# Kernel optimization log

Measured on AMD Instinct MI355X. Metric: run time of the kernel, lower is better.

Reference implementation:

```python
import jax, jax.numpy as jnp
import numpy as np

# ---- config (matches init_kwargs) ----
NUM_HEADS = 8
HEAD_DIM = 48
IN_CH = 384
OUT_CH = 384
AGENTS_HW = (7, 7)
CLUSTERS_HW = (2, 2)
NUM_MODULES = 2          # ['PartitionalClustering', 'FuzzyClustering']
N_GROUPS = 1 + 2 * NUM_MODULES   # p + (k, v) per module
D = NUM_HEADS * HEAD_DIM          # 384
NUM_CLUSTERS = CLUSTERS_HW[0] * CLUSTERS_HW[1]   # 4 per module
NUM_ALL_CLUSTERS = NUM_MODULES * NUM_CLUSTERS    # 8
EPS = 1e-6


def adaptive_avg_pool(x, oh, ow):
    # x: [b, c, H, W], H % oh == 0, W % ow == 0 -> exact block mean
    b, c, H, W = x.shape
    return x.reshape(b, c, oh, H // oh, ow, W // ow).mean(axis=(3, 5))


def setup_inputs() -> dict:
    key = jax.random.key(0)
    ks = jax.random.split(key, 6)
    B, H, W = 16, 56, 56
    x = jax.random.normal(ks[0], (B, IN_CH, H, W), dtype=jnp.float32)
    # proj: 1x1 linear in_channels -> N_GROUPS * D
    proj_w = jax.random.normal(ks[1], (N_GROUPS * D, IN_CH), dtype=jnp.float32) * (IN_CH ** -0.5)
    proj_b = jnp.zeros((N_GROUPS * D,), dtype=jnp.float32)
    sim_alpha = jnp.ones((NUM_ALL_CLUSTERS,), dtype=jnp.float32)
    sim_beta = jnp.zeros((NUM_ALL_CLUSTERS,), dtype=jnp.float32)
    proj2_w = jax.random.normal(ks[2], (OUT_CH, D), dtype=jnp.float32) * (D ** -0.5)
    proj2_b = jnp.zeros((OUT_CH,), dtype=jnp.float32)
    return {"x": x, "proj_w": proj_w, "proj_b": proj_b,
            "sim_alpha": sim_alpha, "sim_beta": sim_beta,
            "proj2_w": proj2_w, "proj2_b": proj2_b}


def _cluster_attention(i, k, v, kc, vc):
    # k: [b, c, Na] agent keys; v: [b, Na, c] agent values
    # kc, vc: [b, M, c] cluster centroids (keys / values)
    c = k.shape[1]
    scores = jnp.einsum('bmc,bcn->bmn', kc, k) / jnp.sqrt(jnp.float32(c))  # [b, M, Na]
    if i == 0:  # PartitionalClustering: attend over tokens per centroid
        attn = jax.nn.softmax(scores, axis=-1)
        agg = jnp.einsum('bmn,bnc->bmc', attn, v)
    else:       # FuzzyClustering: soft membership over clusters, normalized average
        memb = jax.nn.softmax(scores, axis=1)                              # over clusters
        agg = jnp.einsum('bmn,bnc->bmc', memb, v) / (memb.sum(axis=-1, keepdims=True) + EPS)
    return agg + vc  # with_cluster_bias=True


def reference(x, proj_w, proj_b, sim_alpha, sim_beta, proj2_w, proj2_b):
    B, C, H, W = x.shape
    # proj (1x1 linear over channels)
    y = jnp.einsum('bchw,oc->bohw', x, proj_w) + proj_b[None, :, None, None]
    y = y.reshape(B, N_GROUPS, D, H, W).transpose(1, 0, 2, 3, 4)
    b = B * NUM_HEADS
    c = HEAD_DIM
    y = y.reshape(N_GROUPS, b, c, H, W)
    p, r = y[0], y[1:]
    r = r.reshape(NUM_MODULES, 2, b, c, H, W)

    ah, aw = AGENTS_HW
    na = ah * aw
    agg_list = []
    for i in range(NUM_MODULES):  # fixed small structural loop
        k_full, v_full = r[i, 0], r[i, 1]
        kc = adaptive_avg_pool(k_full, *CLUSTERS_HW).reshape(b, c, NUM_CLUSTERS).transpose(0, 2, 1)
        vc = adaptive_avg_pool(v_full, *CLUSTERS_HW).reshape(b, c, NUM_CLUSTERS).transpose(0, 2, 1)
        k = adaptive_avg_pool(k_full, ah, aw).reshape(b, c, na)             # [b, c, Na]
        v = adaptive_avg_pool(v_full, ah, aw).reshape(b, c, na).transpose(0, 2, 1)  # [b, Na, c]
        agg_list.append(_cluster_attention(i, k, v, kc, vc))
    agg = jnp.concatenate(agg_list, axis=1)  # [b, M_all, c]

    p_agents = adaptive_avg_pool(p, ah, aw).reshape(b, c, na)  # [b, c, Na]
    # cosine similarity between centroid aggregates and query tokens
    agg_n = agg / (jnp.linalg.norm(agg, axis=-1, keepdims=True) + EPS)
    p_n = p_agents / (jnp.linalg.norm(p_agents, axis=1, keepdims=True) + EPS)
    sim = jnp.einsum('bmc,bcn->bmn', agg_n, p_n)  # [b, M_all, Na]
    similarity = sim_alpha[None, :, None] * sim + sim_beta[None, :, None]
    assignment = jax.nn.softmax(similarity, axis=1)  # over clusters

    out = jnp.einsum('bmc,bmn->bcn', agg, assignment)  # [b, c, Na]
    out = out.reshape(b, c, ah, aw)
    # bilinear upsample (half-pixel centers == torch align_corners=False)
    out = jax.image.resize(out, (b, c, H, W), method='linear')
    out = out.reshape(B, D, H, W)
    out = jnp.einsum('bdhw,od->bohw', out, proj2_w) + proj2_b[None, :, None, None]
    return out
```

## Files before the change

kernel.cpp:

```cpp
#include <hip/hip_runtime.h>
#include <math.h>

#define CIN    384
#define NPIX   3136

typedef float vf4 __attribute__((ext_vector_type(4)));
typedef __attribute__((ext_vector_type(4))) float f32x4;
typedef __attribute__((ext_vector_type(8))) short bf16x8;
typedef __attribute__((ext_vector_type(8))) unsigned short u16x8;

__device__ __forceinline__ unsigned short f2bf(float f) {
    unsigned u = __float_as_uint(f);
    u = (u + 0x7FFF + ((u >> 16) & 1)) >> 16;
    return (unsigned short)u;
}
__device__ __forceinline__ float bf2f(unsigned short h) {
    return __uint_as_float(((unsigned)h) << 16);
}

__global__ __launch_bounds__(256) void k_front(const float* __restrict__ x,
                                               const float* __restrict__ W1,
                                               const float* __restrict__ W2,
                                               unsigned short* __restrict__ Xhi,
                                               unsigned short* __restrict__ Xlo,
                                               unsigned short* __restrict__ Whi1,
                                               unsigned short* __restrict__ Wlo1,
                                               unsigned short* __restrict__ Whi2,
                                               unsigned short* __restrict__ Wlo2) {
    int blk = blockIdx.x;
    int t = threadIdx.x;
    if (blk >= 9024) {
        int i = (blk - 9024) * 256 + t;
        float w = W2[i];
        unsigned short hi = f2bf(w);
        Whi2[i] = hi;
        Wlo2[i] = f2bf(w - bf2f(hi));
        return;
    }
    if (blk >= 6144) {
        int i = (blk - 6144) * 256 + t;
        float w = W1[i];
        unsigned short hi = f2bf(w);
        Whi1[i] = hi;
        Wlo1[i] = f2bf(w - bf2f(hi));
        return;
    }
    int Bi = blk / CIN;
    int ch = blk - Bi * CIN;
    __shared__ float ps[56][14];
    __shared__ float s14[14][14];
    const float* xp = x + (size_t)(Bi * CIN + ch) * NPIX;
    for (int p = t; p < 784; p += 256) {
        int row = p / 14, cb = p % 14;
        const vf4 v = __builtin_nontemporal_load(
            reinterpret_cast<const vf4*>(xp + row * 56 + cb * 4));
        ps[row][cb] = v.x + v.y + v.z + v.w;
    }
    __syncthreads();
    if (t < 196) {
        int ri = t / 14, cb = t % 14;
        s14[ri][cb] = ps[4*ri][cb] + ps[4*ri+1][cb] + ps[4*ri+2][cb] + ps[4*ri+3][cb];
    }
    __syncthreads();
    if (t < 49) {
        int i = t / 7, j = t % 7;
        float s = (s14[2*i][2*j] + s14[2*i][2*j+1] + s14[2*i+1][2*j] + s14[2*i+1][2*j+1])
                  * (1.0f / 64.0f);
        int p = Bi * 49 + t;
        unsigned short hi = f2bf(s);
        Xhi[(size_t)p * 384 + ch] = hi;
        Xlo[(size_t)p * 384 + ch] = f2bf(s - bf2f(hi));
    } else if (t >= 64 && t < 68) {
        int m = t - 64;
        int mi = m / 2, mj = m % 2;
        float s = 0.f;
        for (int ri = 7*mi; ri < 7*mi + 7; ++ri)
            for (int cb = 7*mj; cb < 7*mj + 7; ++cb)
                s += s14[ri][cb];
        s *= (1.0f / 784.0f);
        int p = 784 + Bi * 4 + m;
        unsigned short hi = f2bf(s);
        Xhi[(size_t)p * 384 + ch] = hi;
        Xlo[(size_t)p * 384 + ch] = f2bf(s - bf2f(hi));
    }
}

__global__ __launch_bounds__(512) void k_fuse(
        const unsigned short* __restrict__ Whi, const unsigned short* __restrict__ Wlo,
        const unsigned short* __restrict__ Xhi, const unsigned short* __restrict__ Xlo,
        const float* __restrict__ proj_b,
        const float* __restrict__ alpha, const float* __restrict__ beta,
        unsigned short* __restrict__ osThi, unsigned short* __restrict__ osTlo) {
    int bb = blockIdx.x;
    int Bi = bb >> 3, head = bb & 7;
    __shared__ float yT[16560];
    __shared__ float e0[4][49], memb[4][49];
    __shared__ float msum[4];
    __shared__ float agg[8][48];
    __shared__ float anorm[8], pnorm[49];
    __shared__ float simL[8][49];
    __shared__ float assignW[8][49];
    unsigned short* sAh = (unsigned short*)yT;
    unsigned short* sAl = sAh + 9600;
    unsigned short* sBh = sAl + 9600;
    unsigned short* sBl = sBh + 2560;
    int t = threadIdx.x;
    int lane = t & 63, w = t >> 6;
    int fr = lane & 15, fq = lane >> 4;

    int row0 = t >> 2, ko0 = (t & 3) * 8;
    int g0 = row0 / 48, cc0 = row0 - g0 * 48;
    size_t aoff0 = (size_t)(g0 * 384 + head * 48 + cc0) * 384 + ko0;
    int c1 = t + 512;
    int row1 = c1 >> 2, ko1 = (c1 & 3) * 8;
    int g1 = row1 / 48, cc1 = row1 - g1 * 48;
    size_t aoff1 = (size_t)(g1 * 384 + head * 48 + cc1) * 384 + ko1;
    int bko = (t & 3) * 8;
    int brow = t >> 2;
    int bp = brow < 49 ? Bi * 49 + brow : 784 + Bi * 4 + (brow - 49);
    size_t boff = (size_t)bp * 384 + bko;

    u16x8 rAh0, rAl0, rAh1, rAl1, rBh, rBl;
    rAh0 = *(const u16x8*)(Whi + aoff0);
    rAl0 = *(const u16x8*)(Wlo + aoff0);
    if (t < 448) { rAh1 = *(const u16x8*)(Whi + aoff1); rAl1 = *(const u16x8*)(Wlo + aoff1); }
    if (t < 212) { rBh  = *(const u16x8*)(Xhi + boff);  rBl  = *(const u16x8*)(Xlo + boff); }

    f32x4 acc[2][4] = {};
    for (int step = 0; step < 12; ++step) {
        *(u16x8*)&sAh[row0 * 40 + ko0] = rAh0;
        *(u16x8*)&sAl[row0 * 40 + ko0] = rAl0;
        if (t < 448) {
            *(u16x8*)&sAh[row1 * 40 + ko1] = rAh1;
            *(u16x8*)&sAl[row1 * 40 + ko1] = rAl1;
        }
        if (t < 212) {
            *(u16x8*)&sBh[brow * 40 + bko] = rBh;
            *(u16x8*)&sBl[brow * 40 + bko] = rBl;
        }
        __syncthreads();
        if (step < 11) {
            int k0 = (step + 1) * 32;
            rAh0 = *(const u16x8*)(Whi + aoff0 + k0);
            rAl0 = *(const u16x8*)(Wlo + aoff0 + k0);
            if (t < 448) { rAh1 = *(const u16x8*)(Whi + aoff1 + k0); rAl1 = *(const u16x8*)(Wlo + aoff1 + k0); }
            if (t < 212) { rBh  = *(const u16x8*)(Xhi + boff + k0);  rBl  = *(const u16x8*)(Xlo + boff + k0); }
        }
        bf16x8 bh[4], bl[4];
#pragma unroll
        for (int nt = 0; nt < 4; ++nt) {
            int r = nt * 16 + fr;
            bh[nt] = *(const bf16x8*)&sBh[r * 40 + fq * 8];
            bl[nt] = *(const bf16x8*)&sBl[r * 40 + fq * 8];
        }
#pragma unroll
        for (int mi = 0; mi < 2; ++mi) {
            int mt = 2 * w + mi;
            if (mt < 15) {
                int r = mt * 16 + fr;
                bf16x8 ah = *(const bf16x8*)&sAh[r * 40 + fq * 8];
                bf16x8 al = *(const bf16x8*)&sAl[r * 40 + fq * 8];
#pragma unroll
                for (int nt = 0; nt < 4; ++nt) {
                    acc[mi][nt] = __builtin_amdgcn_mfma_f32_16x16x32_bf16(ah, bh[nt], acc[mi][nt], 0, 0, 0);
                    acc[mi][nt] = __builtin_amdgcn_mfma_f32_16x16x32_bf16(ah, bl[nt], acc[mi][nt], 0, 0, 0);
                    acc[mi][nt] = __builtin_amdgcn_mfma_f32_16x16x32_bf16(al, bh[nt], acc[mi][nt], 0, 0, 0);
                }
            }
        }
        __syncthreads();
    }
#pragma unroll
    for (int mi = 0; mi < 2; ++mi) {
        int mt = 2 * w + mi;
        if (mt < 15) {
#pragma unroll
            for (int j = 0; j < 4; ++j) {
                int m = mt * 16 + fq * 4 + j;
                int g = m / 48, cc = m - g * 48;
                float bb = proj_b[g * 384 + head * 48 + cc];
#pragma unroll
                for (int nt = 0; nt < 4; ++nt)
                    yT[m * 69 + nt * 16 + fr] = acc[mi][nt][j] + bb;
            }
        }
    }
    __syncthreads();

    const float scale = 0.14433756729740643f;
    if (t < 392) {
        int i = t / 196, r = t % 196;
        int m = r / 49, n = r % 49;
        int rbase = 48 + 96 * i;
        float s = 0.f;
        for (int cc = 0; cc < 48; ++cc)
            s += yT[(rbase + cc) * 69 + 49 + m] * yT[(rbase + cc) * 69 + n];
        s *= scale;
        if (i == 0) e0[m][n] = s; else memb[m][n] = s;
    }
    __syncthreads();
    if (w < 4) {
        float v = (lane < 49) ? e0[w][lane] : -1e30f;
        float mx = v;
#pragma unroll
        for (int off = 32; off; off >>= 1) mx = fmaxf(mx, __shfl_xor(mx, off));
        float e = (lane < 49) ? __expf(v - mx) : 0.f;
        float s = e;
#pragma unroll
        for (int off = 32; off; off >>= 1) s += __shfl_xor(s, off);
        if (lane < 49) e0[w][lane] = e / s;
    } else if (w == 4 && lane < 49) {
        int n = lane;
        float a0 = memb[0][n], a1 = memb[1][n], a2 = memb[2][n], a3 = memb[3][n];
        float mx = fmaxf(fmaxf(a0, a1), fmaxf(a2, a3));
        float x0 = __expf(a0 - mx), x1 = __expf(a1 - mx);
        float x2 = __expf(a2 - mx), x3 = __expf(a3 - mx);
        float s = x0 + x1 + x2 + x3;
        memb[0][n] = x0 / s; memb[1][n] = x1 / s; memb[2][n] = x2 / s; memb[3][n] = x3 / s;
    }
    __syncthreads();
    if (w >= 4) {
        int m = w - 4;
        float v = (lane < 49) ? memb[m][lane] : 0.f;
#pragma unroll
        for (int off = 32; off; off >>= 1) v += __shfl_xor(v, off);
        if (lane == 0) msum[m] = v;
    }
    __syncthreads();
    if (t < 384) {
        int row = t / 48, cc = t % 48;
        float a = 0.f;
        if (row < 4) {
            const float* vr = &yT[(96 + cc) * 69];
            for (int n = 0; n < 49; ++n) a += e0[row][n] * vr[n];
            agg[row][cc] = a + vr[49 + row];
        } else {
            int m = row - 4;
            const float* vr = &yT[(192 + cc) * 69];
            for (int n = 0; n < 49; ++n) a += memb[m][n] * vr[n];
            agg[row][cc] = a / (msum[m] + 1e-6f) + vr[49 + m];
        }
    }
    __syncthreads();
    {
        float v = 0.f;
        if (lane < 48) { float a = agg[w][lane]; v = a * a; }
#pragma unroll
        for (int off = 32; off; off >>= 1) v += __shfl_xor(v, off);
        if (lane == 0) anorm[w] = sqrtf(v) + 1e-6f;
    }
    if (t < 49) {
        int n = t; float s = 0.f;
        for (int cc = 0; cc < 48; ++cc) { float a = yT[cc * 69 + n]; s += a * a; }
        pnorm[n] = sqrtf(s) + 1e-6f;
    }
    __syncthreads();
    if (t < 392) {
        int m = t / 49, n = t - m * 49;
        float dot = 0.f;
        for (int cc = 0; cc < 48; ++cc) dot += agg[m][cc] * yT[cc * 69 + n];
        simL[m][n] = alpha[m] * (dot / (anorm[m] * pnorm[n])) + beta[m];
    }
    __syncthreads();
    if (t < 49) {
        int n = t;
        float mx = -1e30f, e[8];
        for (int m = 0; m < 8; ++m) mx = fmaxf(mx, simL[m][n]);
        float ssum = 0.f;
        for (int m = 0; m < 8; ++m) { e[m] = __expf(simL[m][n] - mx); ssum += e[m]; }
        float inv = 1.f / ssum;
        for (int m = 0; m < 8; ++m) assignW[m][n] = e[m] * inv;
    }
    __syncthreads();
    for (int idx = t; idx < 3072; idx += 512) {
        int n = idx / 48, cc = idx - n * 48;
        float s = 0.f;
        if (n < 49)
            for (int m = 0; m < 8; ++m) s += agg[m][cc] * assignW[m][n];
        size_t o = ((size_t)(Bi * 64 + n)) * 384 + head * 48 + cc;
        unsigned short hi = f2bf(s);
        osThi[o] = hi;
        osTlo[o] = f2bf(s - bf2f(hi));
    }
}

__global__ __launch_bounds__(256) void k_tail(
        const unsigned short* __restrict__ Whi2, const unsigned short* __restrict__ Wlo2,
        const unsigned short* __restrict__ osThi, const unsigned short* __restrict__ osTlo,
        const float* __restrict__ b2, float* __restrict__ out) {
    int blk = blockIdx.x;
    int Bi = blk / 96, cg = blk - Bi * 96;
    int ch0 = cg * 4;
    __shared__ unsigned short sAh[16 * 40], sAl[16 * 40];
    __shared__ unsigned short sBh[64 * 40], sBl[64 * 40];
    __shared__ float zL[4][64];
    __shared__ float tmp[4][56][8];
    int t = threadIdx.x;
    int lane = t & 63, w = t >> 6;
    int fr = lane & 15, fq = lane >> 4;
    for (int idx = t; idx < 480; idx += 256) {
        int r = 4 + idx / 40, c = idx % 40;
        sAh[r * 40 + c] = 0; sAl[r * 40 + c] = 0;
    }
    int brow = t >> 2, bko = (t & 3) * 8;
    size_t boff = ((size_t)(Bi * 64 + brow)) * 384 + bko;
    f32x4 acc = {0, 0, 0, 0};
    for (int k0 = 0; k0 < 384; k0 += 32) {
        if (t < 16) {
            int arow = t >> 2, ako = (t & 3) * 8;
            size_t aoff = (size_t)(ch0 + arow) * 384 + k0 + ako;
            *(u16x8*)&sAh[arow * 40 + ako] = *(const u16x8*)(Whi2 + aoff);
            *(u16x8*)&sAl[arow * 40 + ako] = *(const u16x8*)(Wlo2 + aoff);
        }
        *(u16x8*)&sBh[brow * 40 + bko] = *(const u16x8*)(osThi + boff + k0);
        *(u16x8*)&sBl[brow * 40 + bko] = *(const u16x8*)(osTlo + boff + k0);
        __syncthreads();
        bf16x8 ah = *(const bf16x8*)&sAh[fr * 40 + fq * 8];
        bf16x8 al = *(const bf16x8*)&sAl[fr * 40 + fq * 8];
        int rb = w * 16 + fr;
        bf16x8 bh = *(const bf16x8*)&sBh[rb * 40 + fq * 8];
        bf16x8 bl = *(const bf16x8*)&sBl[rb * 40 + fq * 8];
        acc = __builtin_amdgcn_mfma_f32_16x16x32_bf16(ah, bh, acc, 0, 0, 0);
        acc = __builtin_amdgcn_mfma_f32_16x16x32_bf16(ah, bl, acc, 0, 0, 0);
        acc = __builtin_amdgcn_mfma_f32_16x16x32_bf16(al, bh, acc, 0, 0, 0);
        __syncthreads();
    }
    if (fq == 0) {
#pragma unroll
        for (int j = 0; j < 4; ++j)
            zL[j][w * 16 + fr] = acc[j] + b2[ch0 + j];
    }
    __syncthreads();
    for (int idx = t; idx < 1568; idx += 256) {
        int c = idx / 392, rem = idx - c * 392;
        int h = rem / 7, iw = rem - h * 7;
        float sh = (h - 3.5f) * 0.125f;
        int ih0; float fh;
        if (sh <= 0.f)      { ih0 = 0; fh = 0.f; }
        else if (sh >= 6.f) { ih0 = 6; fh = 0.f; }
        else                { ih0 = (int)sh; fh = sh - (float)ih0; }
        int ih1 = min(ih0 + 1, 6);
        float z0 = zL[c][ih0 * 7 + iw];
        tmp[c][h][iw] = z0 + fh * (zL[c][ih1 * 7 + iw] - z0);
    }
    __syncthreads();
    size_t obase = ((size_t)(Bi * 384 + ch0)) * (size_t)NPIX;
    for (int q = t; q < 3136; q += 256) {
        int c = q / 784, rem = q - c * 784;
        int h = rem / 14, qw = rem - h * 14;
        const float* tr = &tmp[c][h][0];
        vf4 o4;
#pragma unroll
        for (int j = 0; j < 4; ++j) {
            int ww = qw * 4 + j;
            float sw = (ww - 3.5f) * 0.125f;
            int iw0; float fw;
            if (sw <= 0.f)      { iw0 = 0; fw = 0.f; }
            else if (sw >= 6.f) { iw0 = 6; fw = 0.f; }
            else                { iw0 = (int)sw; fw = sw - (float)iw0; }
            int iw1 = min(iw0 + 1, 6);
            float t0 = tr[iw0];
            o4[j] = t0 + fw * (tr[iw1] - t0);
        }
        __builtin_nontemporal_store(o4,
            reinterpret_cast<vf4*>(out + obase + (size_t)q * 4));
    }
}

extern "C" void kernel_launch(void* const* d_in, const int* in_sizes, int n_in,
                              void* d_out, int out_size, void* d_ws, size_t ws_size,
                              hipStream_t stream) {
    const float* x      = (const float*)d_in[0];
    const float* proj_w = (const float*)d_in[1];
    const float* proj_b = (const float*)d_in[2];
    const float* alpha  = (const float*)d_in[3];
    const float* beta   = (const float*)d_in[4];
    const float* w2     = (const float*)d_in[5];
    const float* b2     = (const float*)d_in[6];
    float* out = (float*)d_out;
    float* ws  = (float*)d_ws;

    unsigned short* Whi1  = (unsigned short*)(ws);
    unsigned short* Wlo1  = (unsigned short*)(ws + (size_t)368640);
    unsigned short* Xhi   = (unsigned short*)(ws + (size_t)737280);
    unsigned short* Xlo   = (unsigned short*)(ws + (size_t)909312);
    unsigned short* Whi2  = (unsigned short*)(ws + (size_t)1081344);
    unsigned short* Wlo2  = (unsigned short*)(ws + (size_t)1155072);
    unsigned short* osThi = (unsigned short*)(ws + (size_t)1228800);
    unsigned short* osTlo = (unsigned short*)(ws + (size_t)1425408);

    k_front<<<dim3(9600), 256, 0, stream>>>(x, proj_w, w2, Xhi, Xlo, Whi1, Wlo1, Whi2, Wlo2);
    k_fuse <<<dim3(128),  512, 0, stream>>>(Whi1, Wlo1, Xhi, Xlo, proj_b, alpha, beta, osThi, osTlo);
    k_tail <<<dim3(1536), 256, 0, stream>>>(Whi2, Wlo2, osThi, osTlo, b2, out);
}
```

Before: 73.04 us.

## Add transposed LDS copy for vectorized attention dots; load tail GEMM operands directly

In the fused attention kernel, the projection output is also written to a transposed shared buffer (yN) with padded strides. This lets the key/query, norm and similarity dot products use float4 LDS reads instead of strided scalar reads, and the small loops are unrolled. In the tail kernel, the LDS staging and barriers for the bf16 GEMM operands are removed, and each lane loads its MFMA fragments straight from global memory. The cost is extra shared memory (about 52KB more) plus duplicated stores in the fused kernel, and less coalesced global loads in the tail.

```diff
diff --git a/kernel.cpp b/kernel.cpp
--- a/kernel.cpp
+++ b/kernel.cpp
@@ -16,6 +16,11 @@
 }
 __device__ __forceinline__ float bf2f(unsigned short h) {
     return __uint_as_float(((unsigned)h) << 16);
+}
+__device__ __forceinline__ float dot4(const float* a, const float* b) {
+    float4 x = *reinterpret_cast<const float4*>(a);
+    float4 y = *reinterpret_cast<const float4*>(b);
+    return x.x * y.x + x.y * y.y + x.z * y.z + x.w * y.w;
 }
 
 __global__ __launch_bounds__(256) void k_front(const float* __restrict__ x,
@@ -93,13 +98,14 @@
         unsigned short* __restrict__ osThi, unsigned short* __restrict__ osTlo) {
     int bb = blockIdx.x;
     int Bi = bb >> 3, head = bb & 7;
-    __shared__ float yT[16560];
-    __shared__ float e0[4][49], memb[4][49];
+    __shared__ float yT[240 * 72];
+    __shared__ float yN[53 * 244];
+    __shared__ float e0[4 * 52], memb[4 * 52];
     __shared__ float msum[4];
     __shared__ float agg[8][48];
     __shared__ float anorm[8], pnorm[49];
-    __shared__ float simL[8][49];
-    __shared__ float assignW[8][49];
+    __shared__ float simL[8 * 49];
+    __shared__ float assignW[8 * 49];
     unsigned short* sAh = (unsigned short*)yT;
     unsigned short* sAl = sAh + 9600;
     unsigned short* sBh = sAl + 9600;
@@ -180,8 +186,12 @@
                 int g = m / 48, cc = m - g * 48;
                 float bb = proj_b[g * 384 + head * 48 + cc];
 #pragma unroll
-                for (int nt = 0; nt < 4; ++nt)
-                    yT[m * 69 + nt * 16 + fr] = acc[mi][nt][j] + bb;
+                for (int nt = 0; nt < 4; ++nt) {
+                    int col = nt * 16 + fr;
+                    float v = acc[mi][nt][j] + bb;
+                    yT[m * 72 + col] = v;
+                    if (col < 53) yN[col * 244 + m] = v;
+                }
             }
         }
     }
@@ -191,16 +201,17 @@
     if (t < 392) {
         int i = t / 196, r = t % 196;
         int m = r / 49, n = r % 49;
-        int rbase = 48 + 96 * i;
+        const float* kn = yN + n * 244 + 48 + 96 * i;
+        const float* kc = yN + (49 + m) * 244 + 48 + 96 * i;
         float s = 0.f;
-        for (int cc = 0; cc < 48; ++cc)
-            s += yT[(rbase + cc) * 69 + 49 + m] * yT[(rbase + cc) * 69 + n];
+#pragma unroll
+        for (int j = 0; j < 12; ++j) s += dot4(kc + j * 4, kn + j * 4);
         s *= scale;
-        if (i == 0) e0[m][n] = s; else memb[m][n] = s;
+        if (i == 0) e0[m * 52 + n] = s; else memb[m * 52 + n] = s;
     }
     __syncthreads();
     if (w < 4) {
-        float v = (lane < 49) ? e0[w][lane] : -1e30f;
+        float v = (lane < 49) ? e0[w * 52 + lane] : -1e30f;
         float mx = v;
 #pragma unroll
         for (int off = 32; off; off >>= 1) mx = fmaxf(mx, __shfl_xor(mx, off));
@@ -208,20 +219,20 @@
         float s = e;
 #pragma unroll
         for (int off = 32; off; off >>= 1) s += __shfl_xor(s, off);
-        if (lane < 49) e0[w][lane] = e / s;
+        if (lane < 49) e0[w * 52 + lane] = e / s;
     } else if (w == 4 && lane < 49) {
         int n = lane;
-        float a0 = memb[0][n], a1 = memb[1][n], a2 = memb[2][n], a3 = memb[3][n];
+        float a0 = memb[n], a1 = memb[52 + n], a2 = memb[104 + n], a3 = memb[156 + n];
         float mx = fmaxf(fmaxf(a0, a1), fmaxf(a2, a3));
         float x0 = __expf(a0 - mx), x1 = __expf(a1 - mx);
         float x2 = __expf(a2 - mx), x3 = __expf(a3 - mx);
         float s = x0 + x1 + x2 + x3;
-        memb[0][n] = x0 / s; memb[1][n] = x1 / s; memb[2][n] = x2 / s; memb[3][n] = x3 / s;
+        memb[n] = x0 / s; memb[52 + n] = x1 / s; memb[104 + n] = x2 / s; memb[156 + n] = x3 / s;
     }
     __syncthreads();
     if (w >= 4) {
         int m = w - 4;
-        float v = (lane < 49) ? memb[m][lane] : 0.f;
+        float v = (lane < 49) ? memb[m * 52 + lane] : 0.f;
 #pragma unroll
         for (int off = 32; off; off >>= 1) v += __shfl_xor(v, off);
         if (lane == 0) msum[m] = v;
@@ -231,13 +242,19 @@
         int row = t / 48, cc = t % 48;
         float a = 0.f;
         if (row < 4) {
-            const float* vr = &yT[(96 + cc) * 69];
-            for (int n = 0; n < 49; ++n) a += e0[row][n] * vr[n];
+            const float* vr = yT + (96 + cc) * 72;
+            const float* pe = e0 + row * 52;
+#pragma unroll
+            for (int j = 0; j < 12; ++j) a += dot4(pe + j * 4, vr + j * 4);
+            a += pe[48] * vr[48];
             agg[row][cc] = a + vr[49 + row];
         } else {
             int m = row - 4;
-            const float* vr = &yT[(192 + cc) * 69];
-            for (int n = 0; n < 49; ++n) a += memb[m][n] * vr[n];
+            const float* vr = yT + (192 + cc) * 72;
+            const float* pe = memb + m * 52;
+#pragma unroll
+            for (int j = 0; j < 12; ++j) a += dot4(pe + j * 4, vr + j * 4);
+            a += pe[48] * vr[48];
             agg[row][cc] = a / (msum[m] + 1e-6f) + vr[49 + m];
         }
     }
@@ -250,33 +267,43 @@
         if (lane == 0) anorm[w] = sqrtf(v) + 1e-6f;
     }
     if (t < 49) {
-        int n = t; float s = 0.f;
-        for (int cc = 0; cc < 48; ++cc) { float a = yT[cc * 69 + n]; s += a * a; }
-        pnorm[n] = sqrtf(s) + 1e-6f;
+        const float* pn = yN + t * 244;
+        float s = 0.f;
+#pragma unroll
+        for (int j = 0; j < 12; ++j) s += dot4(pn + j * 4, pn + j * 4);
+        pnorm[t] = sqrtf(s) + 1e-6f;
     }
     __syncthreads();
     if (t < 392) {
         int m = t / 49, n = t - m * 49;
+        const float* am = &agg[m][0];
+        const float* pn = yN + n * 244;
         float dot = 0.f;
-        for (int cc = 0; cc < 48; ++cc) dot += agg[m][cc] * yT[cc * 69 + n];
-        simL[m][n] = alpha[m] * (dot / (anorm[m] * pnorm[n])) + beta[m];
+#pragma unroll
+        for (int j = 0; j < 12; ++j) dot += dot4(am + j * 4, pn + j * 4);
+        simL[m * 49 + n] = alpha[m] * (dot / (anorm[m] * pnorm[n])) + beta[m];
     }
     __syncthreads();
     if (t < 49) {
         int n = t;
         float mx = -1e30f, e[8];
-        for (int m = 0; m < 8; ++m) mx = fmaxf(mx, simL[m][n]);
+#pragma unroll
+        for (int m = 0; m < 8; ++m) mx = fmaxf(mx, simL[m * 49 + n]);
         float ssum = 0.f;
-        for (int m = 0; m < 8; ++m) { e[m] = __expf(simL[m][n] - mx); ssum += e[m]; }
+#pragma unroll
+        for (int m = 0; m < 8; ++m) { e[m] = __expf(simL[m * 49 + n] - mx); ssum += e[m]; }
         float inv = 1.f / ssum;
-        for (int m = 0; m < 8; ++m) assignW[m][n] = e[m] * inv;
+#pragma unroll
+        for (int m = 0; m < 8; ++m) assignW[m * 49 + n] = e[m] * inv;
     }
     __syncthreads();
     for (int idx = t; idx < 3072; idx += 512) {
         int n = idx / 48, cc = idx - n * 48;
         float s = 0.f;
-        if (n < 49)
-            for (int m = 0; m < 8; ++m) s += agg[m][cc] * assignW[m][n];
+        if (n < 49) {
+#pragma unroll
+            for (int m = 0; m < 8; ++m) s += agg[m][cc] * assignW[m * 49 + n];
+        }
         size_t o = ((size_t)(Bi * 64 + n)) * 384 + head * 48 + cc;
         unsigned short hi = f2bf(s);
         osThi[o] = hi;
@@ -291,39 +318,26 @@
     int blk = blockIdx.x;
     int Bi = blk / 96, cg = blk - Bi * 96;
     int ch0 = cg * 4;
-    __shared__ unsigned short sAh[16 * 40], sAl[16 * 40];
-    __shared__ unsigned short sBh[64 * 40], sBl[64 * 40];
     __shared__ float zL[4][64];
     __shared__ float tmp[4][56][8];
     int t = threadIdx.x;
     int lane = t & 63, w = t >> 6;
     int fr = lane & 15, fq = lane >> 4;
-    for (int idx = t; idx < 480; idx += 256) {
-        int r = 4 + idx / 40, c = idx % 40;
-        sAh[r * 40 + c] = 0; sAl[r * 40 + c] = 0;
-    }
-    int brow = t >> 2, bko = (t & 3) * 8;
-    size_t boff = ((size_t)(Bi * 64 + brow)) * 384 + bko;
+    size_t ab = (size_t)(ch0 + fr) * 384 + fq * 8;
+    size_t bb = ((size_t)(Bi * 64 + w * 16 + fr)) * 384 + fq * 8;
     f32x4 acc = {0, 0, 0, 0};
+#pragma unroll
     for (int k0 = 0; k0 < 384; k0 += 32) {
-        if (t < 16) {
-            int arow = t >> 2, ako = (t & 3) * 8;
-            size_t aoff = (size_t)(ch0 + arow) * 384 + k0 + ako;
-            *(u16x8*)&sAh[arow * 40 + ako] = *(const u16x8*)(Whi2 + aoff);
-            *(u16x8*)&sAl[arow * 40 + ako] = *(const u16x8*)(Wlo2 + aoff);
-        }
-        *(u16x8*)&sBh[brow * 40 + bko] = *(const u16x8*)(osThi + boff + k0);
-        *(u16x8*)&sBl[brow * 40 + bko] = *(const u16x8*)(osTlo + boff + k0);
-        __syncthreads();
-        bf16x8 ah = *(const bf16x8*)&sAh[fr * 40 + fq * 8];
-        bf16x8 al = *(const bf16x8*)&sAl[fr * 40 + fq * 8];
-        int rb = w * 16 + fr;
-        bf16x8 bh = *(const bf16x8*)&sBh[rb * 40 + fq * 8];
-        bf16x8 bl = *(const bf16x8*)&sBl[rb * 40 + fq * 8];
+        bf16x8 ah = {0,0,0,0,0,0,0,0}, al = {0,0,0,0,0,0,0,0};
+        if (fr < 4) {
+            ah = *(const bf16x8*)(const void*)(Whi2 + ab + k0);
+            al = *(const bf16x8*)(const void*)(Wlo2 + ab + k0);
+        }
+        bf16x8 bh = *(const bf16x8*)(const void*)(osThi + bb + k0);
+        bf16x8 bl = *(const bf16x8*)(const void*)(osTlo + bb + k0);
         acc = __builtin_amdgcn_mfma_f32_16x16x32_bf16(ah, bh, acc, 0, 0, 0);
         acc = __builtin_amdgcn_mfma_f32_16x16x32_bf16(ah, bl, acc, 0, 0, 0);
         acc = __builtin_amdgcn_mfma_f32_16x16x32_bf16(al, bh, acc, 0, 0, 0);
-        __syncthreads();
     }
     if (fq == 0) {
 #pragma unroll
```

After: 77.05 us. +5.5%, slower.
